# Performance work log

Hardware: AMD Instinct MI355X
Metric: run time of the kernel (lower is better)

## Reference

```python
import jax, jax.numpy as jnp
import numpy as np

SLOPE = 0.2
NEG = -9e15

def setup_inputs() -> dict:
    key = jax.random.key(0)
    k1, k2, k3, k4 = jax.random.split(key, 4)
    N, INP, OUT = 8192, 512, 128
    h = jax.random.normal(k1, (N, INP), dtype=jnp.float32)
    adj = jax.random.randint(k2, (N, N), 0, 2, dtype=jnp.int32)
    W = jax.random.normal(k3, (INP, OUT), dtype=jnp.float32) * (1.0 / np.sqrt(INP))
    a = jax.random.normal(k4, (2 * OUT,), dtype=jnp.float32) * (1.0 / np.sqrt(2 * OUT))
    return {"h": h, "adj": adj, "W": W, "a": a}

def reference(h, adj, W, a):
    OUT = W.shape[1]
    Wh = h @ W                               # [N, out]
    # a . [Wh_i, Wh_j] decomposes into two matvecs (same math as pairwise concat)
    f1 = Wh @ a[:OUT]                        # [N]
    f2 = Wh @ a[OUT:]                        # [N]
    e = jax.nn.leaky_relu(f1[:, None] + f2[None, :], negative_slope=SLOPE)  # [N, N]
    scores = jnp.where(adj > 0, e, NEG)
    attention = jax.nn.softmax(scores, axis=1)
    return attention @ Wh                    # [N, out]
```

## Files before the change

### kernel.cpp

```cpp
#include <hip/hip_runtime.h>

typedef unsigned short u16;
typedef __attribute__((ext_vector_type(8))) short short8v;
typedef __attribute__((ext_vector_type(4))) short short4v;
typedef __attribute__((ext_vector_type(4))) float float4v;
typedef __attribute__((ext_vector_type(4))) int   int4v;

#define N_NODES 8192
#define D_IN    512
#define D_OUT   128
#define SLOPEF  0.2f

static __device__ __forceinline__ float bf2f(u16 u) {
    union { unsigned int i; float f; } v; v.i = ((unsigned int)u) << 16; return v.f;
}
static __device__ __forceinline__ u16 f2bf(float f) {
    union { float f; unsigned int i; } v; v.f = f;
    unsigned int r = v.i + 0x7fff + ((v.i >> 16) & 1);
    return (u16)(r >> 16);
}
static __device__ __forceinline__ void lds_barrier() {
    asm volatile("s_waitcnt lgkmcnt(0)" ::: "memory");
    __builtin_amdgcn_s_barrier();
    asm volatile("" ::: "memory");
}

__global__ __launch_bounds__(256, 2) void k1_proj(
        const float* __restrict__ h, const float* __restrict__ W,
        const float* __restrict__ a, u16* __restrict__ WhT,
        float* __restrict__ f1, float* __restrict__ f2)
{
    __shared__ float hs[16 * D_IN];
    __shared__ float buf[16 * 128];
    __shared__ float part[16][17];
    const int tid = threadIdx.x;
    const int rowbase = blockIdx.x * 16;

    const float4v* hsrc = (const float4v*)(h + (size_t)rowbase * D_IN);
    #pragma unroll
    for (int i = 0; i < 8; i++) {
        *(float4v*)&hs[(tid + 256 * i) * 4] = hsrc[tid + 256 * i];
    }
    __syncthreads();

    const int c  = tid & 127;
    const int rh = tid >> 7;
    float acc[8];
    #pragma unroll
    for (int rr = 0; rr < 8; rr++) acc[rr] = 0.f;

    for (int k = 0; k < D_IN; k += 4) {
        float wv[4];
        #pragma unroll
        for (int kk = 0; kk < 4; kk++) wv[kk] = W[(k + kk) * D_OUT + c];
        #pragma unroll
        for (int rr = 0; rr < 8; rr++) {
            float4v hv = *(const float4v*)&hs[(rh * 8 + rr) * D_IN + k];
            acc[rr] += hv[0] * wv[0];
            acc[rr] += hv[1] * wv[1];
            acc[rr] += hv[2] * wv[2];
            acc[rr] += hv[3] * wv[3];
        }
    }

    {
        short8v pack;
        #pragma unroll
        for (int rr = 0; rr < 8; rr++) pack[rr] = (short)f2bf(acc[rr]);
        *(short8v*)(WhT + (size_t)c * N_NODES + rowbase + rh * 8) = pack;
    }

    const float a1 = a[c];
    const float a2 = a[D_OUT + c];

    #pragma unroll
    for (int rr = 0; rr < 8; rr++) buf[(rh * 8 + rr) * 128 + c] = acc[rr] * a1;
    __syncthreads();
    {
        const int row = tid >> 4, seg = tid & 15;
        float p = 0.f;
        #pragma unroll
        for (int e = 0; e < 8; e++) p += buf[row * 128 + seg * 8 + e];
        part[row][seg] = p;
    }
    __syncthreads();
    if (tid < 16) {
        float s = 0.f;
        #pragma unroll
        for (int j = 0; j < 16; j++) s += part[tid][j];
        f1[rowbase + tid] = s;
    }
    __syncthreads();
    #pragma unroll
    for (int rr = 0; rr < 8; rr++) buf[(rh * 8 + rr) * 128 + c] = acc[rr] * a2;
    __syncthreads();
    {
        const int row = tid >> 4, seg = tid & 15;
        float p = 0.f;
        #pragma unroll
        for (int e = 0; e < 8; e++) p += buf[row * 128 + seg * 8 + e];
        part[row][seg] = p;
    }
    __syncthreads();
    if (tid < 16) {
        float s = 0.f;
        #pragma unroll
        for (int j = 0; j < 16; j++) s += part[tid][j];
        f2[rowbase + tid] = s;
    }
}

__global__ __launch_bounds__(256, 1) void k2_attn(
        const int* __restrict__ adj, const u16* __restrict__ WhT,
        const float* __restrict__ f1g, const float* __restrict__ f2g,
        float* __restrict__ out)
{
    __shared__ short Pt[32 * 264];
    __shared__ float f2s[256];
    __shared__ float f1s[32];
    __shared__ float rs[32][9];
    __shared__ float ssum[32];

    const int tid = threadIdx.x;
    const int rowbase = blockIdx.x * 32;
    const int r = tid >> 3, g = tid & 7;
    const int lane = tid & 63, w = tid >> 6;
    const int quad = lane >> 4, m16 = lane & 15;

    if (tid < 32) f1s[tid] = f1g[rowbase + tid];
    if (tid < 64) *(float4v*)&f2s[tid * 4] = *(const float4v*)&f2g[tid * 4];

    const int4v* arow = (const int4v*)(adj + (size_t)(rowbase + r) * N_NODES);
    int4v a4[8];
    #pragma unroll
    for (int i = 0; i < 8; i++) a4[i] = arow[g + 8 * i];

    float4v acc[2][2];
    #pragma unroll
    for (int mt = 0; mt < 2; mt++)
        #pragma unroll
        for (int nt = 0; nt < 2; nt++) {
            acc[mt][nt][0] = 0.f; acc[mt][nt][1] = 0.f;
            acc[mt][nt][2] = 0.f; acc[mt][nt][3] = 0.f;
        }
    float lsum = 0.f;

    lds_barrier();

    for (int jc = 0; jc < 32; jc++) {
        float4v f2next;
        const bool ldf2 = (jc + 1 < 32) && (tid < 64);
        if (ldf2) f2next = *(const float4v*)&f2g[(jc + 1) * 256 + tid * 4];

        const float f1v = f1s[r];
        #pragma unroll
        for (int i = 0; i < 8; i++) {
            const int c0 = (g + 8 * i) * 4;
            const float4v fv = *(const float4v*)&f2s[c0];
            const int4v av = a4[i];
            short4v pv;
            #pragma unroll
            for (int e = 0; e < 4; e++) {
                float x = f1v + fv[e];
                x = fmaxf(x, SLOPEF * x);
                const float wv = (av[e] > 0) ? __expf(x) : 0.f;
                const u16 wb = f2bf(wv);
                lsum += bf2f(wb);
                pv[e] = (short)wb;
            }
            *(short4v*)&Pt[r * 264 + c0] = pv;
        }
        if (jc + 1 < 32) {
            #pragma unroll
            for (int i = 0; i < 8; i++) a4[i] = arow[(jc + 1) * 64 + g + 8 * i];
        }
        lds_barrier();

        {
            const u16* b0p = WhT + (size_t)(w * 32 + m16) * N_NODES + jc * 256 + quad * 8;
            const u16* b1p = b0p + 16 * N_NODES;
            const short* a0p = &Pt[m16 * 264 + quad * 8];
            const short* a1p = a0p + 16 * 264;
            #pragma unroll
            for (int ks = 0; ks < 8; ks++) {
                const int ko = ks * 32;
                const short8v af0 = *(const short8v*)(a0p + ko);
                const short8v af1 = *(const short8v*)(a1p + ko);
                const short8v bv0 = *(const short8v*)(b0p + ko);
                const short8v bv1 = *(const short8v*)(b1p + ko);
                acc[0][0] = __builtin_amdgcn_mfma_f32_16x16x32_bf16(af0, bv0, acc[0][0], 0, 0, 0);
                acc[0][1] = __builtin_amdgcn_mfma_f32_16x16x32_bf16(af0, bv1, acc[0][1], 0, 0, 0);
                acc[1][0] = __builtin_amdgcn_mfma_f32_16x16x32_bf16(af1, bv0, acc[1][0], 0, 0, 0);
                acc[1][1] = __builtin_amdgcn_mfma_f32_16x16x32_bf16(af1, bv1, acc[1][1], 0, 0, 0);
            }
        }
        if (ldf2) *(float4v*)&f2s[tid * 4] = f2next;
        lds_barrier();
    }

    rs[r][g] = lsum;
    __syncthreads();
    if (tid < 32) {
        float s = 0.f;
        #pragma unroll
        for (int j = 0; j < 8; j++) s += rs[tid][j];
        ssum[tid] = s;
    }
    __syncthreads();

    #pragma unroll
    for (int mt = 0; mt < 2; mt++) {
        #pragma unroll
        for (int nt = 0; nt < 2; nt++) {
            const int cl = w * 32 + nt * 16 + m16;
            #pragma unroll
            for (int reg = 0; reg < 4; reg++) {
                const int rl = mt * 16 + quad * 4 + reg;
                const float val = acc[mt][nt][reg] / ssum[rl];
                out[(size_t)(rowbase + rl) * D_OUT + cl] = val;
            }
        }
    }
}

extern "C" void kernel_launch(void* const* d_in, const int* in_sizes, int n_in,
                              void* d_out, int out_size, void* d_ws, size_t ws_size,
                              hipStream_t stream) {
    const float* h   = (const float*)d_in[0];
    const int*   adj = (const int*)d_in[1];
    const float* W   = (const float*)d_in[2];
    const float* a   = (const float*)d_in[3];

    u16*   WhT = (u16*)d_ws;
    float* f1  = (float*)((char*)d_ws + (size_t)2 * 1024 * 1024);
    float* f2  = f1 + N_NODES;

    k1_proj<<<N_NODES / 16, 256, 0, stream>>>(h, W, a, WhT, f1, f2);
    k2_attn<<<N_NODES / 32, 256, 0, stream>>>(adj, WhT, f1, f2, (float*)d_out);
}
```

Measured before the change: 482.3 us.

## Split attention columns into four segments with a separate reduction kernel

Each row block of the attention kernel is split into four column segments, so four times as many blocks launch and the occupancy hint rises to 4 blocks per CU. Each block writes unnormalized partial numerators and denominators to workspace. A new kernel sums the partials and divides. This targets low occupancy and exposed latency, at the cost of extra partial-result traffic and one more launch.

```diff
diff --git a/kernel.cpp b/kernel.cpp
--- a/kernel.cpp
+++ b/kernel.cpp
@@ -10,6 +10,9 @@
 #define D_IN    512
 #define D_OUT   128
 #define SLOPEF  0.2f
+#define NSEG    4
+#define SEGCOLS 2048
+#define NCHUNK  8
 
 static __device__ __forceinline__ float bf2f(u16 u) {
     union { unsigned int i; float f; } v; v.i = ((unsigned int)u) << 16; return v.f;
@@ -110,27 +113,32 @@
     }
 }
 
-__global__ __launch_bounds__(256, 1) void k2_attn(
+__global__ __launch_bounds__(256, 4) void k2_attn(
         const int* __restrict__ adj, const u16* __restrict__ WhT,
         const float* __restrict__ f1g, const float* __restrict__ f2g,
-        float* __restrict__ out)
+        float* __restrict__ numw, float* __restrict__ denw)
 {
     __shared__ short Pt[32 * 264];
-    __shared__ float f2s[256];
+    __shared__ float f2s[SEGCOLS];
     __shared__ float f1s[32];
     __shared__ float rs[32][9];
     __shared__ float ssum[32];
 
     const int tid = threadIdx.x;
-    const int rowbase = blockIdx.x * 32;
+    const int rb  = blockIdx.x >> 2;
+    const int seg = blockIdx.x & 3;
+    const int rowbase = rb * 32;
+    const int colbase = seg * SEGCOLS;
     const int r = tid >> 3, g = tid & 7;
     const int lane = tid & 63, w = tid >> 6;
     const int quad = lane >> 4, m16 = lane & 15;
 
     if (tid < 32) f1s[tid] = f1g[rowbase + tid];
-    if (tid < 64) *(float4v*)&f2s[tid * 4] = *(const float4v*)&f2g[tid * 4];
-
-    const int4v* arow = (const int4v*)(adj + (size_t)(rowbase + r) * N_NODES);
+    #pragma unroll
+    for (int i = 0; i < 2; i++)
+        *(float4v*)&f2s[(tid + 256 * i) * 4] = *(const float4v*)&f2g[colbase + (tid + 256 * i) * 4];
+
+    const int4v* arow = (const int4v*)(adj + (size_t)(rowbase + r) * N_NODES + colbase);
     int4v a4[8];
     #pragma unroll
     for (int i = 0; i < 8; i++) a4[i] = arow[g + 8 * i];
@@ -145,18 +153,14 @@
         }
     float lsum = 0.f;
 
-    lds_barrier();
-
-    for (int jc = 0; jc < 32; jc++) {
-        float4v f2next;
-        const bool ldf2 = (jc + 1 < 32) && (tid < 64);
-        if (ldf2) f2next = *(const float4v*)&f2g[(jc + 1) * 256 + tid * 4];
-
+    __syncthreads();
+
+    for (int jc = 0; jc < NCHUNK; jc++) {
         const float f1v = f1s[r];
         #pragma unroll
         for (int i = 0; i < 8; i++) {
             const int c0 = (g + 8 * i) * 4;
-            const float4v fv = *(const float4v*)&f2s[c0];
+            const float4v fv = *(const float4v*)&f2s[jc * 256 + c0];
             const int4v av = a4[i];
             short4v pv;
             #pragma unroll
@@ -170,14 +174,14 @@
             }
             *(short4v*)&Pt[r * 264 + c0] = pv;
         }
-        if (jc + 1 < 32) {
+        if (jc + 1 < NCHUNK) {
             #pragma unroll
             for (int i = 0; i < 8; i++) a4[i] = arow[(jc + 1) * 64 + g + 8 * i];
         }
         lds_barrier();
 
         {
-            const u16* b0p = WhT + (size_t)(w * 32 + m16) * N_NODES + jc * 256 + quad * 8;
+            const u16* b0p = WhT + (size_t)(w * 32 + m16) * N_NODES + colbase + jc * 256 + quad * 8;
             const u16* b1p = b0p + 16 * N_NODES;
             const short* a0p = &Pt[m16 * 264 + quad * 8];
             const short* a1p = a0p + 16 * 264;
@@ -194,7 +198,6 @@
                 acc[1][1] = __builtin_amdgcn_mfma_f32_16x16x32_bf16(af1, bv1, acc[1][1], 0, 0, 0);
             }
         }
-        if (ldf2) *(float4v*)&f2s[tid * 4] = f2next;
         lds_barrier();
     }
 
@@ -205,6 +208,7 @@
         #pragma unroll
         for (int j = 0; j < 8; j++) s += rs[tid][j];
         ssum[tid] = s;
+        denw[(size_t)(rowbase + tid) * NSEG + seg] = s;
     }
     __syncthreads();
 
@@ -216,11 +220,26 @@
             #pragma unroll
             for (int reg = 0; reg < 4; reg++) {
                 const int rl = mt * 16 + quad * 4 + reg;
-                const float val = acc[mt][nt][reg] / ssum[rl];
-                out[(size_t)(rowbase + rl) * D_OUT + cl] = val;
+                numw[((size_t)(rowbase + rl) * NSEG + seg) * D_OUT + cl] = acc[mt][nt][reg];
             }
         }
     }
+}
+
+__global__ __launch_bounds__(256) void k3_reduce(
+        const float* __restrict__ numw, const float* __restrict__ denw,
+        float* __restrict__ out)
+{
+    const int tid = threadIdx.x;
+    const int row = blockIdx.x * 2 + (tid >> 7);
+    const int c   = tid & 127;
+    float s = 0.f, d = 0.f;
+    #pragma unroll
+    for (int sg = 0; sg < NSEG; sg++) {
+        s += numw[((size_t)row * NSEG + sg) * D_OUT + c];
+        d += denw[(size_t)row * NSEG + sg];
+    }
+    out[(size_t)row * D_OUT + c] = s / d;
 }
 
 extern "C" void kernel_launch(void* const* d_in, const int* in_sizes, int n_in,
@@ -231,10 +250,14 @@
     const float* W   = (const float*)d_in[2];
     const float* a   = (const float*)d_in[3];
 
-    u16*   WhT = (u16*)d_ws;
-    float* f1  = (float*)((char*)d_ws + (size_t)2 * 1024 * 1024);
+    char* ws = (char*)d_ws;
+    u16*   WhT = (u16*)ws;
+    float* f1  = (float*)(ws + (size_t)2 * 1024 * 1024);
     float* f2  = f1 + N_NODES;
+    float* numw = (float*)(ws + (size_t)4 * 1024 * 1024);
+    float* denw = (float*)(ws + (size_t)20 * 1024 * 1024);
 
     k1_proj<<<N_NODES / 16, 256, 0, stream>>>(h, W, a, WhT, f1, f2);
-    k2_attn<<<N_NODES / 32, 256, 0, stream>>>(adj, WhT, f1, f2, (float*)d_out);
-}
+    k2_attn<<<(N_NODES / 32) * NSEG, 256, 0, stream>>>(adj, WhT, f1, f2, numw, denw);
+    k3_reduce<<<N_NODES / 2, 256, 0, stream>>>(numw, denw, (float*)d_out);
+}
```

After: 434.1 us. 10.0% less time.
